# Optimization experiments

Hardware: AMD Instinct MI355X
Metric: run time of the kernel (lower is better)

Reference implementation:

```python
import jax, jax.numpy as jnp
import numpy as np

B, S, D, H, L, FFN = 32, 512, 512, 8, 4, 1024
DH = D // H
EPS = 1e-5


def make_pe(seq, d):
    pos = np.arange(seq)[:, None].astype(np.float64)
    i = np.arange(d)[None, :]
    angle = pos / np.power(10000.0, (i // 2 * 2.0) / d)
    pe = angle.copy()
    pe[:, 0::2] = np.sin(angle[:, 0::2])
    pe[:, 1::2] = np.cos(angle[:, 1::2])
    return jnp.asarray(pe, dtype=jnp.float32)


def layer_norm(x, g, b):
    mu = jnp.mean(x, axis=-1, keepdims=True)
    var = jnp.mean((x - mu) ** 2, axis=-1, keepdims=True)
    return (x - mu) * jax.lax.rsqrt(var + EPS) * g + b


def setup_inputs() -> dict:
    key = jax.random.key(0)
    ks = jax.random.split(key, 12)
    sd = 0.02
    d = {
        "x": jax.random.normal(ks[0], (B, S, D), dtype=jnp.float32),
        "pe": make_pe(S, D),
        "Wq": jax.random.normal(ks[1], (L, D, D), dtype=jnp.float32) * sd,
        "bq": jnp.zeros((L, D), dtype=jnp.float32),
        "Wk": jax.random.normal(ks[2], (L, D, D), dtype=jnp.float32) * sd,
        "bk": jnp.zeros((L, D), dtype=jnp.float32),
        "Wv": jax.random.normal(ks[3], (L, D, D), dtype=jnp.float32) * sd,
        "bv": jnp.zeros((L, D), dtype=jnp.float32),
        "Wo": jax.random.normal(ks[4], (L, D, D), dtype=jnp.float32) * sd,
        "bo": jnp.zeros((L, D), dtype=jnp.float32),
        "ln1_g": jnp.ones((L, D), dtype=jnp.float32),
        "ln1_b": jnp.zeros((L, D), dtype=jnp.float32),
        "W1": jax.random.normal(ks[5], (L, D, FFN), dtype=jnp.float32) * sd,
        "b1": jnp.zeros((L, FFN), dtype=jnp.float32),
        "W2": jax.random.normal(ks[6], (L, FFN, D), dtype=jnp.float32) * sd,
        "b2": jnp.zeros((L, D), dtype=jnp.float32),
        "ln2_g": jnp.ones((L, D), dtype=jnp.float32),
        "ln2_b": jnp.zeros((L, D), dtype=jnp.float32),
    }
    return d


def reference(x, pe, Wq, bq, Wk, bk, Wv, bv, Wo, bo, ln1_g, ln1_b,
              W1, b1, W2, b2, ln2_g, ln2_b):
    out = x + pe  # positional encoding (dropout = identity in eval)
    scale = DH ** (-0.5)
    for l in range(L):
        # projections (B,S,D)
        Q = out @ Wq[l] + bq[l]
        K = out @ Wk[l] + bk[l]
        V = out @ Wv[l] + bv[l]
        # faithful raw view (no head transpose), matching torch .view semantics
        Qh = Q.reshape(B * H, S, DH)
        Kh = K.reshape(B * H, S, DH)
        Vh = V.reshape(B * H, S, DH)
        att = jnp.einsum('bqd,bkd->bqk', Qh, Kh) * scale  # (B*H,S,S)
        att = jax.nn.softmax(att, axis=-1)
        ctx = jnp.einsum('bqk,bkd->bqd', att, Vh).reshape(B, S, D)
        a = layer_norm(ctx @ Wo[l] + bo[l] + out, ln1_g[l], ln1_b[l])
        # position-wise FFN
        h = jax.nn.relu(a @ W1[l] + b1[l])
        out = layer_norm(h @ W2[l] + b2[l] + a, ln2_g[l], ln2_b[l])
    return out.reshape(B, S * D)
```

## Files before the change

kernel.cpp:

```cpp
#include <hip/hip_runtime.h>
#include <stdint.h>

#define NB 32
#define NS 512
#define ND 512
#define NH 8
#define NL 4
#define NF 1024
#define NDH 64
#define NM (NB*NS)
#define WLSTRIDE 2097152

typedef __attribute__((ext_vector_type(8))) short bf16x8;
typedef __attribute__((ext_vector_type(4))) short s16x4;
typedef __attribute__((ext_vector_type(4))) float f32x4;

#define VM0  asm volatile("s_waitcnt vmcnt(0)" ::: "memory")
#define VM4  asm volatile("s_waitcnt vmcnt(4)" ::: "memory")
#define VM8  asm volatile("s_waitcnt vmcnt(8)" ::: "memory")
#define SCHB __builtin_amdgcn_sched_barrier(0)
#define SB   __builtin_amdgcn_s_barrier()

__device__ __forceinline__ short f2bf(float f) {
    union { float f; uint32_t u; } v; v.f = f;
    uint32_t r = (v.u + 0x7FFFu + ((v.u >> 16) & 1u)) >> 16;
    return (short)r;
}
__device__ __forceinline__ float bf2f(short s) {
    union { uint32_t u; float f; } v; v.u = ((uint32_t)(uint16_t)s) << 16;
    return v.f;
}
__device__ __forceinline__ f32x4 mfma16(bf16x8 a, bf16x8 b, f32x4 c) {
    return __builtin_amdgcn_mfma_f32_16x16x32_bf16(a, b, c, 0, 0, 0);
}
__device__ __forceinline__ void gld16(const void* g, void* l) {
    __builtin_amdgcn_global_load_lds(
        (const __attribute__((address_space(1))) void*)g,
        (__attribute__((address_space(3))) void*)l, 16, 0, 0);
}
__device__ __forceinline__ void xcd_swz(int& bx, int& by, int gx, int gy) {
    int n = gx * gy;
    int f = by * gx + bx;
    int q = n >> 3;
    int xcd = f & 7, idx = f >> 3;
    int s = xcd * q + idx;
    bx = s % gx; by = s / gx;
}

__global__ __launch_bounds__(256) void convT_k(const float* __restrict__ src,
        short* __restrict__ dst, int K, int N, int woff)
{
    __shared__ float T[64][65];
    int tk = K >> 6, tn = N >> 6;
    int bid = blockIdx.x;
    int l = bid / (tk * tn), rb = bid % (tk * tn);
    int k0 = (rb / tn) << 6, n0 = (rb % tn) << 6;
    const float* s = src + (size_t)l * K * N;
    short* d = dst + (size_t)l * WLSTRIDE + woff;
    int tr = threadIdx.x >> 4, tc = threadIdx.x & 15;
    #pragma unroll
    for (int p = 0; p < 4; p++) {
        int row = p * 16 + tr;
        f32x4 v = *(const f32x4*)(s + (size_t)(k0 + row) * N + n0 + tc * 4);
        #pragma unroll
        for (int j = 0; j < 4; j++) T[row][tc * 4 + j] = v[j];
    }
    __syncthreads();
    #pragma unroll
    for (int p = 0; p < 4; p++) {
        int nrow = p * 16 + tr;
        s16x4 w;
        #pragma unroll
        for (int j = 0; j < 4; j++) w[j] = f2bf(T[tc * 4 + j][nrow]);
        *(s16x4*)(d + (size_t)(n0 + nrow) * K + k0 + tc * 4) = w;
    }
}

__global__ __launch_bounds__(256) void biaspack_k(const float* __restrict__ bq,
        const float* __restrict__ bk, const float* __restrict__ bv, float* __restrict__ out)
{
    int i = blockIdx.x * 256 + threadIdx.x;
    if (i >= NL * 1536) return;
    int l = i / 1536, j = i - l * 1536;
    float v = (j < 512) ? bq[l * 512 + j] : (j < 1024) ? bk[l * 512 + j - 512]
                                                       : bv[l * 512 + j - 1024];
    out[i] = v;
}

__global__ __launch_bounds__(256) void addpe_k(const float* __restrict__ x,
        const float* __restrict__ pe, short* __restrict__ X)
{
    size_t i = ((size_t)blockIdx.x * 256 + threadIdx.x) * 8;
    size_t sd = i % (size_t)(NS * ND);
    f32x4 a0 = *(const f32x4*)(x + i);
    f32x4 a1 = *(const f32x4*)(x + i + 4);
    f32x4 p0 = *(const f32x4*)(pe + sd);
    f32x4 p1 = *(const f32x4*)(pe + sd + 4);
    bf16x8 r;
    #pragma unroll
    for (int j = 0; j < 4; j++) { r[j] = f2bf(a0[j] + p0[j]); r[4 + j] = f2bf(a1[j] + p1[j]); }
    *(bf16x8*)(X + i) = r;
}

template<int EPI>
__global__ __launch_bounds__(256) void gemm_bt(
        const short* __restrict__ A, const short* __restrict__ Bt,
        const float* __restrict__ bias, const short* __restrict__ res,
        void* __restrict__ C0, void* __restrict__ C1, void* __restrict__ C2,
        int M, int N, int K)
{
    __shared__ __align__(16) short Al[16384];
    __shared__ __align__(16) short Bl[16384];
    const int tid = threadIdx.x;
    const int wid = tid >> 6, lane = tid & 63;
    int bx = blockIdx.x, by = blockIdx.y;
    xcd_swz(bx, by, gridDim.x, gridDim.y);
    const int m0 = by * 128, n0 = bx * 128;
    const int wr = wid >> 1, wc = wid & 1;

    f32x4 acc[4][4];
    f32x4 zz = {0.f, 0.f, 0.f, 0.f};
    #pragma unroll
    for (int i = 0; i < 4; i++)
        #pragma unroll
        for (int j = 0; j < 4; j++) acc[i][j] = zz;

    const size_t rk = (size_t)K * 2;
    const char* Ab = (const char*)A + (size_t)m0 * rk;
    const char* Bb = (const char*)Bt + (size_t)n0 * rk;

    int srow[4], scol[4];
    #pragma unroll
    for (int c = 0; c < 4; c++) {
        int p = c * 4096 + tid * 16;
        int l = p ^ (((p >> 7) & 7) << 4);
        srow[c] = l >> 7;  scol[c] = l & 127;
    }

    auto stage = [&](int dofs, int kt) {
        size_t kb = (size_t)(kt << 6) * 2;
        #pragma unroll
        for (int c = 0; c < 4; c++)
            gld16(Ab + (size_t)srow[c] * rk + kb + scol[c],
                  (char*)Al + dofs + c * 4096 + wid * 1024);
        #pragma unroll
        for (int c = 0; c < 4; c++)
            gld16(Bb + (size_t)srow[c] * rk + kb + scol[c],
                  (char*)Bl + dofs + c * 4096 + wid * 1024);
    };
    auto compute = [&](int dofs) {
        #pragma unroll
        for (int ks = 0; ks < 2; ks++) {
            bf16x8 af[4], bfr[4];
            #pragma unroll
            for (int mf = 0; mf < 4; mf++) {
                int row = wr * 64 + mf * 16 + (lane & 15);
                int off = (row * 128 + ks * 64 + ((lane >> 4) * 16)) ^ ((row & 7) << 4);
                af[mf] = *(const bf16x8*)((const char*)Al + dofs + off);
            }
            #pragma unroll
            for (int nf = 0; nf < 4; nf++) {
                int row = wc * 64 + nf * 16 + (lane & 15);
                int off = (row * 128 + ks * 64 + ((lane >> 4) * 16)) ^ ((row & 7) << 4);
                bfr[nf] = *(const bf16x8*)((const char*)Bl + dofs + off);
            }
            #pragma unroll
            for (int mf = 0; mf < 4; mf++)
                #pragma unroll
                for (int nf = 0; nf < 4; nf++)
                    acc[mf][nf] = mfma16(af[mf], bfr[nf], acc[mf][nf]);
        }
    };

    const int nt = K >> 6;
    stage(0, 0);
    stage(16384, 1);
    VM8; SCHB; SB;
    for (int t = 0; t < nt; t += 2) {
        compute(0);
        SB;
        if (t + 2 < nt) { stage(0, t + 2); VM8; } else VM0;
        SCHB; SB;
        compute(16384);
        SB;
        if (t + 3 < nt) { stage(16384, t + 3); VM8; } else VM0;
        SCHB; SB;
    }

    void* outp;
    int colbase, ostride;
    if (EPI == 0) {
        int seg = n0 >> 9;
        outp = (seg == 0) ? C0 : (seg == 1) ? C1 : C2;
        colbase = n0 & 511; ostride = 512;
    } else {
        outp = C0; colbase = n0; ostride = N;
    }

    #pragma unroll
    for (int mf = 0; mf < 4; mf++) {
        #pragma unroll
        for (int nf = 0; nf < 4; nf++) {
            int colg = n0 + wc * 64 + nf * 16 + (lane & 15);
            int col  = colbase + wc * 64 + nf * 16 + (lane & 15);
            float bi = bias[colg];
            #pragma unroll
            for (int r = 0; r < 4; r++) {
                int row = m0 + wr * 64 + mf * 16 + ((lane >> 4) << 2) + r;
                float v = acc[mf][nf][r] + bi;
                if (EPI == 0) {
                    ((short*)outp)[(size_t)row * 512 + col] = f2bf(v);
                } else if (EPI == 1) {
                    ((short*)outp)[(size_t)row * ostride + col] = f2bf(fmaxf(v, 0.f));
                } else {
                    v += bf2f(res[(size_t)row * ostride + col]);
                    ((float*)outp)[(size_t)row * ostride + col] = v;
                }
            }
        }
    }
}

__global__ __launch_bounds__(256) void vtrans_k(const short* __restrict__ V,
        short* __restrict__ VT)
{
    __shared__ short T[64][65];
    const int tid = threadIdx.x;
    const int r0 = blockIdx.x * 64, g = blockIdx.y;
    const size_t base = (size_t)g * 32768;
    #pragma unroll
    for (int rep = 0; rep < 2; rep++) {
        int chunk = rep * 256 + tid;
        int sr = chunk >> 3, c8 = (chunk & 7) * 8;
        bf16x8 v = *(const bf16x8*)(V + base + (size_t)(r0 + sr) * 64 + c8);
        #pragma unroll
        for (int j = 0; j < 8; j++) T[sr][c8 + j] = v[j];
    }
    __syncthreads();
    #pragma unroll
    for (int rep = 0; rep < 2; rep++) {
        int chunk = rep * 256 + tid;
        int dh = chunk >> 3, c8 = (chunk & 7) * 8;
        bf16x8 w;
        #pragma unroll
        for (int j = 0; j < 8; j++) w[j] = T[c8 + j][dh];
        *(bf16x8*)(VT + base + (size_t)dh * 512 + r0 + c8) = w;
    }
}

__global__ __launch_bounds__(256) void attn_k(
        const short* __restrict__ Q, const short* __restrict__ Kb,
        const short* __restrict__ VT, short* __restrict__ ctx)
{
    __shared__ __align__(16) short Kl[8192];
    __shared__ __align__(16) short Vl[8192];
    __shared__ __align__(16) short Pl[8192];
    const int tid = threadIdx.x, wid = tid >> 6, lane = tid & 63;
    int bx = blockIdx.x, by = blockIdx.y;
    xcd_swz(bx, by, gridDim.x, gridDim.y);
    const int g = by, q0 = bx * 128;
    const size_t base = (size_t)g * 32768;
    const float C = 0.18033688f;

    bf16x8 qa[2][2];
    #pragma unroll
    for (int qf = 0; qf < 2; qf++)
        #pragma unroll
        for (int ks = 0; ks < 2; ks++)
            qa[qf][ks] = *(const bf16x8*)(Q + base
                + (size_t)(q0 + wid * 32 + qf * 16 + (lane & 15)) * 64
                + ks * 32 + ((lane >> 4) * 8));

    f32x4 o[2][4];
    float ps[2][4];
    f32x4 zz = {0.f, 0.f, 0.f, 0.f};
    #pragma unroll
    for (int qf = 0; qf < 2; qf++) {
        #pragma unroll
        for (int nf = 0; nf < 4; nf++) o[qf][nf] = zz;
        #pragma unroll
        for (int r = 0; r < 4; r++) ps[qf][r] = 0.f;
    }

    const char* Kbase = (const char*)(Kb + base);
    const char* Vbase = (const char*)(VT + base);

    int ksp[2], srow[2], scol[2];
    #pragma unroll
    for (int c = 0; c < 2; c++) {
        int p = c * 4096 + tid * 16;
        ksp[c] = p ^ (((p >> 7) & 7) << 4);
        srow[c] = ksp[c] >> 7;  scol[c] = ksp[c] & 127;
    }

    auto stage = [&](int dofs, int kt) {
        #pragma unroll
        for (int c = 0; c < 2; c++)
            gld16(Kbase + (size_t)kt * 8192 + ksp[c],
                  (char*)Kl + dofs + c * 4096 + wid * 1024);
        #pragma unroll
        for (int c = 0; c < 2; c++)
            gld16(Vbase + (size_t)srow[c] * 1024 + kt * 128 + scol[c],
                  (char*)Vl + dofs + c * 4096 + wid * 1024);
    };

    auto tile = [&](int dofs) {
        f32x4 sc[2][4];
        #pragma unroll
        for (int qf = 0; qf < 2; qf++)
            #pragma unroll
            for (int nf = 0; nf < 4; nf++) sc[qf][nf] = zz;
        #pragma unroll
        for (int ks = 0; ks < 2; ks++) {
            #pragma unroll
            for (int nf = 0; nf < 4; nf++) {
                int kvr = nf * 16 + (lane & 15);
                int bo = ((kvr * 128 + ks * 64 + ((lane >> 4) * 16)) ^ ((kvr & 7) << 4)) + dofs;
                bf16x8 kf = *(const bf16x8*)((const char*)Kl + bo);
                #pragma unroll
                for (int qf = 0; qf < 2; qf++)
                    sc[qf][nf] = mfma16(qa[qf][ks], kf, sc[qf][nf]);
            }
        }
        #pragma unroll
        for (int qf = 0; qf < 2; qf++) {
            #pragma unroll
            for (int r = 0; r < 4; r++) {
                int qr = wid * 32 + qf * 16 + ((lane >> 4) << 2) + r;
                float s4 = 0.f;
                #pragma unroll
                for (int nf = 0; nf < 4; nf++) {
                    float p = __builtin_amdgcn_exp2f(sc[qf][nf][r] * C);
                    s4 += p;
                    int bo = (qr * 128 + (nf * 16 + (lane & 15)) * 2) ^ ((qr & 7) << 4);
                    *(short*)((char*)Pl + bo) = f2bf(p);
                }
                ps[qf][r] += s4;
            }
        }
        #pragma unroll
        for (int ks = 0; ks < 2; ks++) {
            bf16x8 pa[2];
            #pragma unroll
            for (int qf = 0; qf < 2; qf++) {
                int qrb = wid * 32 + qf * 16 + (lane & 15);
                int bo = (qrb * 128 + ks * 64 + ((lane >> 4) * 16)) ^ ((qrb & 7) << 4);
                pa[qf] = *(const bf16x8*)((const char*)Pl + bo);
            }
            #pragma unroll
            for (int nf = 0; nf < 4; nf++) {
                int dh = nf * 16 + (lane & 15);
                int bo2 = ((dh * 128 + ks * 64 + ((lane >> 4) * 16)) ^ ((dh & 7) << 4)) + dofs;
                bf16x8 vf = *(const bf16x8*)((const char*)Vl + bo2);
                #pragma unroll
                for (int qf = 0; qf < 2; qf++)
                    o[qf][nf] = mfma16(pa[qf], vf, o[qf][nf]);
            }
        }
    };

    stage(0, 0);
    stage(8192, 1);
    VM4; SCHB; SB;
    for (int kt = 0; kt < 8; kt += 2) {
        tile(0);
        SB;
        if (kt + 2 < 8) { stage(0, kt + 2); VM4; } else VM0;
        SCHB; SB;
        tile(8192);
        SB;
        if (kt + 3 < 8) { stage(8192, kt + 3); VM4; } else VM0;
        SCHB; SB;
    }

    #pragma unroll
    for (int qf = 0; qf < 2; qf++) {
        #pragma unroll
        for (int r = 0; r < 4; r++) {
            float s = ps[qf][r];
            s += __shfl_xor(s, 1);
            s += __shfl_xor(s, 2);
            s += __shfl_xor(s, 4);
            s += __shfl_xor(s, 8);
            float inv = 1.f / s;
            int qr = q0 + wid * 32 + qf * 16 + ((lane >> 4) << 2) + r;
            #pragma unroll
            for (int nf = 0; nf < 4; nf++) {
                int dh = nf * 16 + (lane & 15);
                ctx[base + (size_t)qr * 64 + dh] = f2bf(o[qf][nf][r] * inv);
            }
        }
    }
}

template<int OUTF32>
__global__ __launch_bounds__(256) void ln_k(
        const float* __restrict__ pre, const float* __restrict__ g,
        const float* __restrict__ b, void* __restrict__ out)
{
    int row = blockIdx.x * 4 + (threadIdx.x >> 6);
    int lane = threadIdx.x & 63;
    const float* x = pre + (size_t)row * ND + lane * 8;
    f32x4 a0 = *(const f32x4*)x;
    f32x4 a1 = *(const f32x4*)(x + 4);
    float s = 0.f, sq = 0.f;
    #pragma unroll
    for (int j = 0; j < 4; j++) { s += a0[j]; sq += a0[j] * a0[j]; s += a1[j]; sq += a1[j] * a1[j]; }
    #pragma unroll
    for (int d = 1; d < 64; d <<= 1) { s += __shfl_xor(s, d); sq += __shfl_xor(sq, d); }
    float mean = s * (1.f / ND);
    float var = sq * (1.f / ND) - mean * mean;
    float rstd = rsqrtf(var + 1e-5f);
    const float* gp = g + lane * 8;
    const float* bp = b + lane * 8;
    if (OUTF32) {
        float* op = (float*)out + (size_t)row * ND + lane * 8;
        f32x4 r0, r1;
        #pragma unroll
        for (int j = 0; j < 4; j++) {
            r0[j] = (a0[j] - mean) * rstd * gp[j] + bp[j];
            r1[j] = (a1[j] - mean) * rstd * gp[4 + j] + bp[4 + j];
        }
        *(f32x4*)op = r0;
        *(f32x4*)(op + 4) = r1;
    } else {
        bf16x8 rr;
        #pragma unroll
        for (int j = 0; j < 4; j++) {
            rr[j]     = f2bf((a0[j] - mean) * rstd * gp[j] + bp[j]);
            rr[4 + j] = f2bf((a1[j] - mean) * rstd * gp[4 + j] + bp[4 + j]);
        }
        *(bf16x8*)((short*)out + (size_t)row * ND + lane * 8) = rr;
    }
}

extern "C" void kernel_launch(void* const* d_in, const int* in_sizes, int n_in,
                              void* d_out, int out_size, void* d_ws, size_t ws_size,
                              hipStream_t stream)
{
    (void)in_sizes; (void)n_in; (void)out_size; (void)ws_size;
    const float* x   = (const float*)d_in[0];
    const float* pe  = (const float*)d_in[1];
    const float* Wq  = (const float*)d_in[2];
    const float* bq  = (const float*)d_in[3];
    const float* Wk  = (const float*)d_in[4];
    const float* bk  = (const float*)d_in[5];
    const float* Wv  = (const float*)d_in[6];
    const float* bv  = (const float*)d_in[7];
    const float* Wo  = (const float*)d_in[8];
    const float* bo  = (const float*)d_in[9];
    const float* g1  = (const float*)d_in[10];
    const float* be1 = (const float*)d_in[11];
    const float* W1  = (const float*)d_in[12];
    const float* b1  = (const float*)d_in[13];
    const float* W2  = (const float*)d_in[14];
    const float* b2  = (const float*)d_in[15];
    const float* g2  = (const float*)d_in[16];
    const float* be2 = (const float*)d_in[17];

    char* ws = (char*)d_ws;
    const size_t MB = 1048576;
    short* WT   = (short*)(ws);
    short* XB   = (short*)(ws + 16 * MB);
    short* QB   = (short*)(ws + 32 * MB);
    short* KB   = (short*)(ws + 48 * MB);
    short* VB   = (short*)(ws + 64 * MB);
    short* VTb  = (short*)(ws + 80 * MB);
    short* CT   = (short*)(ws + 96 * MB);
    float* BQKV = (float*)(ws + 112 * MB);
    short* AB   = QB;
    float* PR   = (float*)KB;
    short* HB   = VTb;

    convT_k<<<dim3(NL*8*8),  256, 0, stream>>>(Wq, WT, ND, ND, 0);
    convT_k<<<dim3(NL*8*8),  256, 0, stream>>>(Wk, WT, ND, ND, 262144);
    convT_k<<<dim3(NL*8*8),  256, 0, stream>>>(Wv, WT, ND, ND, 524288);
    convT_k<<<dim3(NL*8*8),  256, 0, stream>>>(Wo, WT, ND, ND, 786432);
    convT_k<<<dim3(NL*8*16), 256, 0, stream>>>(W1, WT, ND, NF, 1048576);
    convT_k<<<dim3(NL*16*8), 256, 0, stream>>>(W2, WT, NF, ND, 1572864);
    biaspack_k<<<dim3(24), 256, 0, stream>>>(bq, bk, bv, BQKV);

    addpe_k<<<dim3(4096), 256, 0, stream>>>(x, pe, XB);

    for (int l = 0; l < NL; l++) {
        const short* wl = WT + (size_t)l * WLSTRIDE;
        gemm_bt<0><<<dim3(12, 128), 256, 0, stream>>>(XB, wl, BQKV + l*1536, nullptr,
                                                      QB, KB, VB, NM, 1536, ND);
        vtrans_k<<<dim3(8, 256), 256, 0, stream>>>(VB, VTb);
        attn_k<<<dim3(4, 256), 256, 0, stream>>>(QB, KB, VTb, CT);
        gemm_bt<2><<<dim3(4, 128), 256, 0, stream>>>(CT, wl + 786432, bo + l*ND, XB,
                                                     PR, nullptr, nullptr, NM, ND, ND);
        ln_k<0><<<dim3(4096), 256, 0, stream>>>(PR, g1 + l*ND, be1 + l*ND, AB);
        gemm_bt<1><<<dim3(8, 128), 256, 0, stream>>>(AB, wl + 1048576, b1 + l*NF, nullptr,
                                                     HB, nullptr, nullptr, NM, NF, ND);
        gemm_bt<2><<<dim3(4, 128), 256, 0, stream>>>(HB, wl + 1572864, b2 + l*ND, AB,
                                                     PR, nullptr, nullptr, NM, ND, NF);
        if (l < NL - 1)
            ln_k<0><<<dim3(4096), 256, 0, stream>>>(PR, g2 + l*ND, be2 + l*ND, XB);
        else
            ln_k<1><<<dim3(4096), 256, 0, stream>>>(PR, g2 + l*ND, be2 + l*ND, (float*)d_out);
    }
}
```

Before: 780.6 us.

## Fold softmax scale into Q projection and pack P stores with permuted key layout

Moves the softmax log2-scaled factor into the QKV GEMM epilogue and the Q bias, so attention computes exp2 directly on raw scores without a multiply. The K tile is read with a permuted row mapping, so each lane's four score columns are contiguous. This allows P to be written to LDS as one 8-byte packed store built with v_cvt_pk_bf16_f32 instead of four scalar bf16 stores. The K staging swizzle is changed to match, which risks LDS bank conflicts or layout mismatch if the permutation is not consistent with the P·V read path.

```diff
diff --git a/kernel.cpp b/kernel.cpp
--- a/kernel.cpp
+++ b/kernel.cpp
@@ -10,10 +10,12 @@
 #define NDH 64
 #define NM (NB*NS)
 #define WLSTRIDE 2097152
+#define CSCALE 0.18033688f
 
 typedef __attribute__((ext_vector_type(8))) short bf16x8;
 typedef __attribute__((ext_vector_type(4))) short s16x4;
 typedef __attribute__((ext_vector_type(4))) float f32x4;
+typedef __attribute__((ext_vector_type(2))) uint32_t u32x2;
 
 #define VM0  asm volatile("s_waitcnt vmcnt(0)" ::: "memory")
 #define VM4  asm volatile("s_waitcnt vmcnt(4)" ::: "memory")
@@ -37,6 +39,11 @@
     __builtin_amdgcn_global_load_lds(
         (const __attribute__((address_space(1))) void*)g,
         (__attribute__((address_space(3))) void*)l, 16, 0, 0);
+}
+__device__ __forceinline__ uint32_t cvtpk(float a, float b) {
+    uint32_t w;
+    asm("v_cvt_pk_bf16_f32 %0, %1, %2" : "=v"(w) : "v"(a), "v"(b));
+    return w;
 }
 __device__ __forceinline__ void xcd_swz(int& bx, int& by, int gx, int gy) {
     int n = gx * gy;
@@ -82,8 +89,8 @@
     int i = blockIdx.x * 256 + threadIdx.x;
     if (i >= NL * 1536) return;
     int l = i / 1536, j = i - l * 1536;
-    float v = (j < 512) ? bq[l * 512 + j] : (j < 1024) ? bk[l * 512 + j - 512]
-                                                       : bv[l * 512 + j - 1024];
+    float v = (j < 512) ? bq[l * 512 + j] * CSCALE
+            : (j < 1024) ? bk[l * 512 + j - 512] : bv[l * 512 + j - 1024];
     out[i] = v;
 }
 
@@ -187,10 +194,11 @@
         SCHB; SB;
     }
 
+    int seg = 0;
     void* outp;
     int colbase, ostride;
     if (EPI == 0) {
-        int seg = n0 >> 9;
+        seg = n0 >> 9;
         outp = (seg == 0) ? C0 : (seg == 1) ? C1 : C2;
         colbase = n0 & 511; ostride = 512;
     } else {
@@ -207,7 +215,9 @@
             #pragma unroll
             for (int r = 0; r < 4; r++) {
                 int row = m0 + wr * 64 + mf * 16 + ((lane >> 4) << 2) + r;
-                float v = acc[mf][nf][r] + bi;
+                float v;
+                if (EPI == 0 && seg == 0) v = acc[mf][nf][r] * CSCALE + bi;
+                else                      v = acc[mf][nf][r] + bi;
                 if (EPI == 0) {
                     ((short*)outp)[(size_t)row * 512 + col] = f2bf(v);
                 } else if (EPI == 1) {
@@ -260,7 +270,6 @@
     xcd_swz(bx, by, gridDim.x, gridDim.y);
     const int g = by, q0 = bx * 128;
     const size_t base = (size_t)g * 32768;
-    const float C = 0.18033688f;
 
     bf16x8 qa[2][2];
     #pragma unroll
@@ -289,8 +298,9 @@
     #pragma unroll
     for (int c = 0; c < 2; c++) {
         int p = c * 4096 + tid * 16;
-        ksp[c] = p ^ (((p >> 7) & 7) << 4);
-        srow[c] = ksp[c] >> 7;  scol[c] = ksp[c] & 127;
+        ksp[c] = p ^ (((p >> 9) & 7) << 4);
+        int pv = p ^ (((p >> 7) & 7) << 4);
+        srow[c] = pv >> 7;  scol[c] = pv & 127;
     }
 
     auto stage = [&](int dofs, int kt) {
@@ -314,30 +324,34 @@
         for (int ks = 0; ks < 2; ks++) {
             #pragma unroll
             for (int nf = 0; nf < 4; nf++) {
-                int kvr = nf * 16 + (lane & 15);
-                int bo = ((kvr * 128 + ks * 64 + ((lane >> 4) * 16)) ^ ((kvr & 7) << 4)) + dofs;
+                int kvr = (lane & 15) * 4 + nf;
+                int bo = (kvr * 128 + ((ks * 64 + ((lane >> 4) * 16)) ^ (((kvr >> 2) & 7) << 4)))
+                         + dofs;
                 bf16x8 kf = *(const bf16x8*)((const char*)Kl + bo);
                 #pragma unroll
                 for (int qf = 0; qf < 2; qf++)
                     sc[qf][nf] = mfma16(qa[qf][ks], kf, sc[qf][nf]);
             }
         }
+
         #pragma unroll
         for (int qf = 0; qf < 2; qf++) {
             #pragma unroll
             for (int r = 0; r < 4; r++) {
                 int qr = wid * 32 + qf * 16 + ((lane >> 4) << 2) + r;
-                float s4 = 0.f;
-                #pragma unroll
-                for (int nf = 0; nf < 4; nf++) {
-                    float p = __builtin_amdgcn_exp2f(sc[qf][nf][r] * C);
-                    s4 += p;
-                    int bo = (qr * 128 + (nf * 16 + (lane & 15)) * 2) ^ ((qr & 7) << 4);
-                    *(short*)((char*)Pl + bo) = f2bf(p);
-                }
-                ps[qf][r] += s4;
-            }
-        }
+                float e0 = __builtin_amdgcn_exp2f(sc[qf][0][r]);
+                float e1 = __builtin_amdgcn_exp2f(sc[qf][1][r]);
+                float e2 = __builtin_amdgcn_exp2f(sc[qf][2][r]);
+                float e3 = __builtin_amdgcn_exp2f(sc[qf][3][r]);
+                ps[qf][r] += (e0 + e1) + (e2 + e3);
+                u32x2 w;
+                w[0] = cvtpk(e0, e1);
+                w[1] = cvtpk(e2, e3);
+                int bo = (qr * 128 + (lane & 15) * 8) ^ ((qr & 7) << 4);
+                *(u32x2*)((char*)Pl + bo) = w;
+            }
+        }
+
         #pragma unroll
         for (int ks = 0; ks < 2; ks++) {
             bf16x8 pa[2];
```

New measurement: 760.0 us. 2.6% less time.
